# Kernel optimization log

Hardware: AMD Instinct MI355X
Metric: run time of the kernel (lower is better)

Reference implementation:

```python
import jax, jax.numpy as jnp
import numpy as np

N_EMBED = 384
HEAD_SIZE = 64
B, T = 128, 512


def rope(x):
    # Faithful to source: fres = 1/1000**(arange(0,dim,2)//dim) -> integer
    # floor-div makes the exponent all zeros, so fres == 1 everywhere.
    Bx, Tx, D = x.shape
    half = D // 2
    fres = jnp.ones((half,), dtype=jnp.float32)
    ang = jnp.arange(Tx, dtype=jnp.float32)[:, None] * fres[None, :]  # (T, half)
    cos, sin = jnp.cos(ang), jnp.sin(ang)
    xr = x.reshape(Bx, Tx, half, 2)
    xe, xo = xr[..., 0], xr[..., 1]
    oe = xe * cos - xo * sin
    oo = xe * sin + xo * cos
    return jnp.stack([oe, oo], axis=-1).reshape(Bx, Tx, D)


def setup_inputs() -> dict:
    key = jax.random.key(0)
    ks = jax.random.split(key, 7)
    s = 1.0 / np.sqrt(N_EMBED)
    return {
        "x": jax.random.normal(ks[0], (B, T, N_EMBED), dtype=jnp.float32),
        "wq": jax.random.uniform(ks[1], (N_EMBED, HEAD_SIZE), jnp.float32, -s, s),
        "bq": jax.random.uniform(ks[2], (HEAD_SIZE,), jnp.float32, -s, s),
        "wk": jax.random.uniform(ks[3], (N_EMBED, HEAD_SIZE), jnp.float32, -s, s),
        "bk": jax.random.uniform(ks[4], (HEAD_SIZE,), jnp.float32, -s, s),
        "wv": jax.random.uniform(ks[5], (N_EMBED, HEAD_SIZE), jnp.float32, -s, s),
        "bv": jax.random.uniform(ks[6], (HEAD_SIZE,), jnp.float32, -s, s),
    }


def reference(x, wq, bq, wk, bk, wv, bv):
    Bx, Tx, C = x.shape  # C = n_embed; scale uses C per the source (not head_size)
    q = rope(x @ wq + bq)
    k = rope(x @ wk + bk)
    wei = jnp.einsum("bqd,bkd->bqk", q, k) * (C ** -0.5)  # (B, T, T)
    causal = jnp.tril(jnp.ones((Tx, Tx), dtype=bool))
    wei = jnp.where(causal, wei, -jnp.inf)
    wei = jax.nn.softmax(wei, axis=-1)
    v = x @ wv + bv
    return jnp.einsum("bqk,bkd->bqd", wei, v)
```

## Files before the change

kernel.cpp:

```cpp
#include <hip/hip_runtime.h>

#define TSEQ 512
#define NB   128
#define CDIM 384
#define HD   64
#define QSCALE 0.051031036307982884f
#define MBIAS  8.0f

typedef _Float16 half8  __attribute__((ext_vector_type(8)));
typedef _Float16 half4  __attribute__((ext_vector_type(4)));
typedef float    floatx4 __attribute__((ext_vector_type(4)));

typedef __attribute__((address_space(3))) unsigned int lds_u32;
typedef const __attribute__((address_space(1))) unsigned int g_u32;

__device__ __forceinline__ void load_lds16(const void* g, void* l) {
    __builtin_amdgcn_global_load_lds((g_u32*)g, (lds_u32*)l, 16, 0, 0);
}

__global__ void prep_w(const float* __restrict__ wq, const float* __restrict__ wk,
                       const float* __restrict__ wv, _Float16* __restrict__ Wp)
{
    int i = blockIdx.x * 256 + threadIdx.x;
    if (i >= 3 * CDIM * HD) return;
    int c    = i / 6144;  int r  = i - c * 6144;
    int kblk = r / 1536;  int r2 = r - kblk * 1536;
    int n    = r2 >> 3;   int kin = r2 & 7;
    int k    = c * 32 + kblk * 8 + kin;
    int mat  = n / 64;    int col = n - mat * 64;
    const float* w = (mat == 0) ? wq : ((mat == 1) ? wk : wv);
    Wp[i] = (_Float16)w[k * HD + col];
}

__global__ __launch_bounds__(256) void qkv_gemm(
    const float* __restrict__ x, const _Float16* __restrict__ Wp,
    const float* __restrict__ bq, const float* __restrict__ bk,
    const float* __restrict__ bv,
    _Float16* __restrict__ Qw, _Float16* __restrict__ Kw,
    _Float16* __restrict__ Vtw, int b0)
{
    __shared__ __align__(16) float    xs[2][64 * 32];
    __shared__ __align__(16) _Float16 wsb[2][6144];

    const int tid  = threadIdx.x;
    const int wave = tid >> 6;
    const int lane = tid & 63;
    const int l16  = lane & 15;
    const int quad = lane >> 4;

    const int row0 = blockIdx.x * 64;
    const size_t rowg = (size_t)b0 * TSEQ + row0;

    const int xr = lane >> 3;
    const int xu = lane & 7;
    size_t xoff[2];
#pragma unroll
    for (int i = 0; i < 2; ++i) {
        const int m = (wave * 2 + i) * 8 + xr;
        xoff[i] = (rowg + m) * CDIM + (size_t)((xu ^ xr) << 2);
    }
    int woff[3];
#pragma unroll
    for (int i = 0; i < 3; ++i) woff[i] = (wave * 3 + i) * 512 + lane * 8;

    floatx4 acc[12];
#pragma unroll
    for (int i = 0; i < 12; ++i)
#pragma unroll
        for (int r = 0; r < 4; ++r) acc[i][r] = 0.f;

#define STAGE(cc, bi) do {                                                    \
    _Pragma("unroll")                                                         \
    for (int i_ = 0; i_ < 2; ++i_)                                            \
        load_lds16(x + xoff[i_] + (cc) * 32,                                  \
                   (char*)&xs[bi][0] + (wave * 2 + i_) * 1024);               \
    _Pragma("unroll")                                                         \
    for (int i_ = 0; i_ < 3; ++i_)                                            \
        load_lds16(Wp + (cc) * 6144 + woff[i_],                               \
                   (char*)&wsb[bi][0] + (wave * 3 + i_) * 1024);              \
} while (0)

    STAGE(0, 0);
    __syncthreads();

#pragma unroll
    for (int c = 0; c < 12; ++c) {
        if (c < 11) STAGE(c + 1, (c + 1) & 1);

        const float*    xb = xs[c & 1];
        const _Float16* wb = wsb[c & 1];
        const int m  = wave * 16 + l16;
        const int mh = l16 & 7;
        const int j0 = quad * 2;
        floatx4 a0 = *(const floatx4*)(xb + m * 32 + ((j0 ^ mh) << 2));
        floatx4 a1 = *(const floatx4*)(xb + m * 32 + (((j0 + 1) ^ mh) << 2));
        half8 a;
#pragma unroll
        for (int jj = 0; jj < 8; ++jj)
            a[jj] = (_Float16)(jj < 4 ? a0[jj] : a1[jj - 4]);
        const _Float16* bp = wb + ((size_t)quad * 192 + l16) * 8;
#pragma unroll
        for (int i = 0; i < 12; ++i) {
            half8 bb = *(const half8*)(bp + i * 128);
            acc[i] = __builtin_amdgcn_mfma_f32_16x16x32_f16(a, bb, acc[i], 0, 0, 0);
        }
        __syncthreads();
    }
#undef STAGE

    float bq4[4], bk4[4], bv4[4];
#pragma unroll
    for (int s4 = 0; s4 < 4; ++s4) {
        const int cc = s4 * 16 + l16;
        bq4[s4] = bq[cc]; bk4[s4] = bk[cc]; bv4[s4] = bv[cc];
    }
    const int t00  = (row0 & (TSEQ - 1)) + wave * 16 + quad * 4;
    const int bidx = row0 >> 9;
    const int rowb = row0 + wave * 16 + quad * 4;

#pragma unroll
    for (int r = 0; r < 4; ++r) {
        const int t = t00 + r;
        const float st = sinf((float)t);
        const float ct = cosf((float)t);
        const int row = rowb + r;
#pragma unroll
        for (int s4 = 0; s4 < 4; ++s4) {
            const int cc = s4 * 16 + l16;
            float vq = acc[s4][r] + bq4[s4];
            float pq = __shfl_xor(vq, 1);
            vq = (cc & 1) ? (pq * st + vq * ct) : (vq * ct - pq * st);
            Qw[(size_t)row * HD + cc] = (_Float16)(vq * QSCALE);
            float vk = acc[4 + s4][r] + bk4[s4];
            float pk = __shfl_xor(vk, 1);
            vk = (cc & 1) ? (pk * st + vk * ct) : (vk * ct - pk * st);
            Kw[(size_t)row * HD + cc] = (_Float16)vk;
        }
    }
#pragma unroll
    for (int s4 = 0; s4 < 4; ++s4) {
        const int cc = s4 * 16 + l16;
        half4 vpack;
#pragma unroll
        for (int r = 0; r < 4; ++r) vpack[r] = (_Float16)(acc[8 + s4][r] + bv4[s4]);
        *(half4*)(Vtw + ((size_t)bidx * HD + cc) * TSEQ + t00) = vpack;
    }
}

__global__ __launch_bounds__(256) void attn_kernel(
    const _Float16* __restrict__ Qw, const _Float16* __restrict__ Kw,
    const _Float16* __restrict__ Vtw, float* __restrict__ out, int b0)
{
    int bx, bl;
    {
        const int lin = blockIdx.y * 8 + blockIdx.x;
        if ((gridDim.y & 7) == 0) {
            const int per = gridDim.y >> 3;
            const int xcd = lin & 7;
            const int k2  = lin >> 3;
            bl = xcd * per + (k2 >> 3);
            bx = k2 & 7;
        } else { bx = blockIdx.x; bl = blockIdx.y; }
    }
    const int tid  = threadIdx.x;
    const int wave = tid >> 6;
    const int lane = tid & 63;
    const int l16  = lane & 15;
    const int quad = lane >> 4;

    const int pr  = bx * 2 + (wave & 1);
    const int h   = wave >> 1;
    const int qA  = pr * 16;
    const int qB  = (31 - pr) * 16;
    const int jdA = pr >> 2;
    const int jdB = (31 - pr) >> 2;

    __shared__ __align__(16) _Float16 pbuf[4][16][72];
    __shared__ __align__(16) floatx4  mbuf[2][10][64];

    const _Float16* Qb = Qw  + (size_t)bl * TSEQ * HD;
    const _Float16* Kb = Kw  + (size_t)bl * TSEQ * HD;
    const _Float16* Vb = Vtw + (size_t)bl * HD * TSEQ;

    half8 aQA0 = *(const half8*)(Qb + (size_t)(qA + l16) * HD + quad * 8);
    half8 aQA1 = *(const half8*)(Qb + (size_t)(qA + l16) * HD + 32 + quad * 8);
    half8 aQB0 = *(const half8*)(Qb + (size_t)(qB + l16) * HD + quad * 8);
    half8 aQB1 = *(const half8*)(Qb + (size_t)(qB + l16) * HD + 32 + quad * 8);

    half8 ones;
#pragma unroll
    for (int jj = 0; jj < 8; ++jj) ones[jj] = (_Float16)1.f;

    floatx4 accO[8], accL[2];
#pragma unroll
    for (int i = 0; i < 8; ++i)
#pragma unroll
        for (int r = 0; r < 4; ++r) accO[i][r] = 0.f;
#pragma unroll
    for (int s = 0; s < 2; ++s)
#pragma unroll
        for (int r = 0; r < 4; ++r) accL[s][r] = 0.f;

    for (int j = h; j <= jdB; j += 2) {
        const int kb = j * 64;

        half8 bK0[4], bK1[4], bV0[4], bV1[4];
#pragma unroll
        for (int s4 = 0; s4 < 4; ++s4) {
            const _Float16* kp = Kb + (size_t)(kb + s4 * 16 + l16) * HD + quad * 8;
            bK0[s4] = *(const half8*)(kp);
            bK1[s4] = *(const half8*)(kp + 32);
            const _Float16* vp = Vb + (size_t)(s4 * 16 + l16) * TSEQ + kb + quad * 8;
            bV0[s4] = *(const half8*)(vp);
            bV1[s4] = *(const half8*)(vp + 32);
        }

        if (j <= jdA) {
            floatx4 st4[4];
            __builtin_amdgcn_s_setprio(1);
#pragma unroll
            for (int s4 = 0; s4 < 4; ++s4) {
#pragma unroll
                for (int r = 0; r < 4; ++r) st4[s4][r] = 0.f;
                st4[s4] = __builtin_amdgcn_mfma_f32_16x16x32_f16(bK0[s4], aQA0, st4[s4], 0, 0, 0);
                st4[s4] = __builtin_amdgcn_mfma_f32_16x16x32_f16(bK1[s4], aQA1, st4[s4], 0, 0, 0);
            }
            __builtin_amdgcn_s_setprio(0);
            const int qrow = qA + l16;
#pragma unroll
            for (int s4 = 0; s4 < 4; ++s4) {
                half4 w;
#pragma unroll
                for (int r = 0; r < 4; ++r) {
                    float p = __expf(fminf(st4[s4][r], 18.f) - MBIAS);
                    if (j == jdA) {
                        const int kcol = kb + s4 * 16 + quad * 4 + r;
                        if (kcol > qrow) p = 0.f;
                    }
                    w[r] = (_Float16)p;
                }
                *(half4*)(&pbuf[wave][l16][s4 * 16 + quad * 4]) = w;
            }
            half8 aP0 = *(const half8*)(&pbuf[wave][l16][quad * 8]);
            half8 aP1 = *(const half8*)(&pbuf[wave][l16][32 + quad * 8]);
            __builtin_amdgcn_s_setprio(1);
#pragma unroll
            for (int s4 = 0; s4 < 4; ++s4) {
                accO[s4] = __builtin_amdgcn_mfma_f32_16x16x32_f16(aP0, bV0[s4], accO[s4], 0, 0, 0);
                accO[s4] = __builtin_amdgcn_mfma_f32_16x16x32_f16(aP1, bV1[s4], accO[s4], 0, 0, 0);
            }
            accL[0] = __builtin_amdgcn_mfma_f32_16x16x32_f16(aP0, ones, accL[0], 0, 0, 0);
            accL[0] = __builtin_amdgcn_mfma_f32_16x16x32_f16(aP1, ones, accL[0], 0, 0, 0);
            __builtin_amdgcn_s_setprio(0);
        }

        {
            floatx4 st4[4];
            __builtin_amdgcn_s_setprio(1);
#pragma unroll
            for (int s4 = 0; s4 < 4; ++s4) {
#pragma unroll
                for (int r = 0; r < 4; ++r) st4[s4][r] = 0.f;
                st4[s4] = __builtin_amdgcn_mfma_f32_16x16x32_f16(bK0[s4], aQB0, st4[s4], 0, 0, 0);
                st4[s4] = __builtin_amdgcn_mfma_f32_16x16x32_f16(bK1[s4], aQB1, st4[s4], 0, 0, 0);
            }
            __builtin_amdgcn_s_setprio(0);
            const int qrow = qB + l16;
#pragma unroll
            for (int s4 = 0; s4 < 4; ++s4) {
                half4 w;
#pragma unroll
                for (int r = 0; r < 4; ++r) {
                    float p = __expf(fminf(st4[s4][r], 18.f) - MBIAS);
                    if (j == jdB) {
                        const int kcol = kb + s4 * 16 + quad * 4 + r;
                        if (kcol > qrow) p = 0.f;
                    }
                    w[r] = (_Float16)p;
                }
                *(half4*)(&pbuf[wave][l16][s4 * 16 + quad * 4]) = w;
            }
            half8 aP0 = *(const half8*)(&pbuf[wave][l16][quad * 8]);
            half8 aP1 = *(const half8*)(&pbuf[wave][l16][32 + quad * 8]);
            __builtin_amdgcn_s_setprio(1);
#pragma unroll
            for (int s4 = 0; s4 < 4; ++s4) {
                accO[4 + s4] = __builtin_amdgcn_mfma_f32_16x16x32_f16(aP0, bV0[s4], accO[4 + s4], 0, 0, 0);
                accO[4 + s4] = __builtin_amdgcn_mfma_f32_16x16x32_f16(aP1, bV1[s4], accO[4 + s4], 0, 0, 0);
            }
            accL[1] = __builtin_amdgcn_mfma_f32_16x16x32_f16(aP0, ones, accL[1], 0, 0, 0);
            accL[1] = __builtin_amdgcn_mfma_f32_16x16x32_f16(aP1, ones, accL[1], 0, 0, 0);
            __builtin_amdgcn_s_setprio(0);
        }
    }

    const int slot = wave & 1;
    if (h == 1) {
#pragma unroll
        for (int i = 0; i < 8; ++i) mbuf[slot][i][lane] = accO[i];
        mbuf[slot][8][lane] = accL[0];
        mbuf[slot][9][lane] = accL[1];
    }
    __syncthreads();
    if (h == 1) return;

#pragma unroll
    for (int i = 0; i < 8; ++i) {
        floatx4 t = mbuf[slot][i][lane];
#pragma unroll
        for (int r = 0; r < 4; ++r) accO[i][r] += t[r];
    }
    {
        floatx4 t8 = mbuf[slot][8][lane];
        floatx4 t9 = mbuf[slot][9][lane];
#pragma unroll
        for (int r = 0; r < 4; ++r) { accL[0][r] += t8[r]; accL[1][r] += t9[r]; }
    }

#pragma unroll
    for (int s = 0; s < 2; ++s) {
        const int qbase = (s == 0) ? qA : qB;
        float inv[4];
#pragma unroll
        for (int r = 0; r < 4; ++r) inv[r] = 1.f / accL[s][r];
#pragma unroll
        for (int s4 = 0; s4 < 4; ++s4) {
            const int dcol = s4 * 16 + l16;
#pragma unroll
            for (int r = 0; r < 4; ++r) {
                const int qr = qbase + quad * 4 + r;
                out[((size_t)(b0 + bl) * TSEQ + qr) * HD + dcol] =
                    accO[s * 4 + s4][r] * inv[r];
            }
        }
    }
}

extern "C" void kernel_launch(void* const* d_in, const int* in_sizes, int n_in,
                              void* d_out, int out_size, void* d_ws, size_t ws_size,
                              hipStream_t stream)
{
    char* ws = (char*)d_ws;
    _Float16* Wp = (_Float16*)ws;
    char* qkv_base = ws + 147456;

    const size_t per_b = (size_t)3 * TSEQ * HD * sizeof(_Float16);
    size_t avail = (ws_size > (size_t)147456) ? ws_size - 147456 : per_b;
    int nbc = (int)(avail / per_b);
    if (nbc > NB) nbc = NB;
    if (nbc < 1)  nbc = 1;

    const size_t chunk_elems = (size_t)nbc * TSEQ * HD;
    _Float16* Qw  = (_Float16*)qkv_base;
    _Float16* Kw  = Qw + chunk_elems;
    _Float16* Vtw = Kw + chunk_elems;

    prep_w<<<dim3((3 * CDIM * HD + 255) / 256), dim3(256), 0, stream>>>(
        (const float*)d_in[1], (const float*)d_in[3], (const float*)d_in[5], Wp);

    for (int b0 = 0; b0 < NB; b0 += nbc) {
        const int nb = (NB - b0 < nbc) ? (NB - b0) : nbc;
        qkv_gemm<<<dim3(nb * 8), dim3(256), 0, stream>>>(
            (const float*)d_in[0], Wp, (const float*)d_in[2], (const float*)d_in[4],
            (const float*)d_in[6], Qw, Kw, Vtw, b0);
        attn_kernel<<<dim3(8, nb), dim3(256), 0, stream>>>(
            Qw, Kw, Vtw, (float*)d_out, b0);
    }
}
```

Before: 210.6 us.

## Double tile rows in QKV GEMM with register x loads; prefetch K/V in attention

The QKV GEMM now computes 128 rows per block, two 16-row groups per wave. x is loaded straight into registers with a register double buffer instead of staging through LDS, and W is staged through a triple-buffered LDS ring using explicit vmcnt waits and raw barriers. The attention loop is software-pipelined so the K/V fragments for the next tile are loaded while the current one is processed, and attn_kernel gets a launch bound asking for two blocks per CU. This is meant to hide global load latency and reuse W across more rows, at the cost of more registers and fewer GEMM blocks.

Result: slower. 220.5 us (+4.7%).

```diff
diff --git a/kernel.cpp b/kernel.cpp
--- a/kernel.cpp
+++ b/kernel.cpp
@@ -39,8 +39,7 @@
     _Float16* __restrict__ Qw, _Float16* __restrict__ Kw,
     _Float16* __restrict__ Vtw, int b0)
 {
-    __shared__ __align__(16) float    xs[2][64 * 32];
-    __shared__ __align__(16) _Float16 wsb[2][6144];
+    __shared__ __align__(16) _Float16 wsb[3][6144];
 
     const int tid  = threadIdx.x;
     const int wave = tid >> 6;
@@ -48,65 +47,77 @@
     const int l16  = lane & 15;
     const int quad = lane >> 4;
 
-    const int row0 = blockIdx.x * 64;
+    const int row0 = blockIdx.x * 128;
     const size_t rowg = (size_t)b0 * TSEQ + row0;
 
-    const int xr = lane >> 3;
-    const int xu = lane & 7;
-    size_t xoff[2];
-#pragma unroll
-    for (int i = 0; i < 2; ++i) {
-        const int m = (wave * 2 + i) * 8 + xr;
-        xoff[i] = (rowg + m) * CDIM + (size_t)((xu ^ xr) << 2);
-    }
     int woff[3];
 #pragma unroll
     for (int i = 0; i < 3; ++i) woff[i] = (wave * 3 + i) * 512 + lane * 8;
 
-    floatx4 acc[12];
-#pragma unroll
-    for (int i = 0; i < 12; ++i)
-#pragma unroll
-        for (int r = 0; r < 4; ++r) acc[i][r] = 0.f;
-
-#define STAGE(cc, bi) do {                                                    \
+    const float* xp[2];
+#pragma unroll
+    for (int g = 0; g < 2; ++g)
+        xp[g] = x + (rowg + wave * 32 + g * 16 + l16) * CDIM + quad * 8;
+
+    floatx4 acc[2][12];
+#pragma unroll
+    for (int g = 0; g < 2; ++g)
+#pragma unroll
+        for (int i = 0; i < 12; ++i)
+#pragma unroll
+            for (int r = 0; r < 4; ++r) acc[g][i][r] = 0.f;
+
+    floatx4 xA[2][2], xB[2][2];
+
+#define WSTAGE(cc) do { _Pragma("unroll")                                     \
+    for (int i_ = 0; i_ < 3; ++i_)                                            \
+        load_lds16(Wp + (size_t)(cc) * 6144 + woff[i_],                       \
+                   (char*)&wsb[(cc) % 3][0] + (wave * 3 + i_) * 1024);        \
+} while (0)
+
+#define XLOAD(cc, S) do { _Pragma("unroll")                                   \
+    for (int g_ = 0; g_ < 2; ++g_) {                                          \
+        S[g_][0] = *(const floatx4*)(xp[g_] + (cc) * 32);                     \
+        S[g_][1] = *(const floatx4*)(xp[g_] + (cc) * 32 + 4);                 \
+    }                                                                         \
+} while (0)
+
+#define CHUNK(cc, CUR, NXT, VM) do {                                          \
+    if ((cc) + 2 < 12) WSTAGE((cc) + 2);                                      \
+    if ((cc) + 1 < 12) XLOAD((cc) + 1, NXT);                                  \
+    asm volatile("s_waitcnt vmcnt(" VM ")" ::: "memory");                     \
+    half8 aF[2];                                                              \
     _Pragma("unroll")                                                         \
-    for (int i_ = 0; i_ < 2; ++i_)                                            \
-        load_lds16(x + xoff[i_] + (cc) * 32,                                  \
-                   (char*)&xs[bi][0] + (wave * 2 + i_) * 1024);               \
+    for (int g_ = 0; g_ < 2; ++g_) {                                          \
+        _Pragma("unroll")                                                     \
+        for (int jj = 0; jj < 8; ++jj)                                        \
+            aF[g_][jj] = (_Float16)(jj < 4 ? CUR[g_][0][jj]                   \
+                                           : CUR[g_][1][jj - 4]);             \
+    }                                                                         \
+    const _Float16* bp = &wsb[(cc) % 3][0] + ((size_t)quad * 192 + l16) * 8;  \
     _Pragma("unroll")                                                         \
-    for (int i_ = 0; i_ < 3; ++i_)                                            \
-        load_lds16(Wp + (cc) * 6144 + woff[i_],                               \
-                   (char*)&wsb[bi][0] + (wave * 3 + i_) * 1024);              \
-} while (0)
-
-    STAGE(0, 0);
-    __syncthreads();
-
-#pragma unroll
-    for (int c = 0; c < 12; ++c) {
-        if (c < 11) STAGE(c + 1, (c + 1) & 1);
-
-        const float*    xb = xs[c & 1];
-        const _Float16* wb = wsb[c & 1];
-        const int m  = wave * 16 + l16;
-        const int mh = l16 & 7;
-        const int j0 = quad * 2;
-        floatx4 a0 = *(const floatx4*)(xb + m * 32 + ((j0 ^ mh) << 2));
-        floatx4 a1 = *(const floatx4*)(xb + m * 32 + (((j0 + 1) ^ mh) << 2));
-        half8 a;
-#pragma unroll
-        for (int jj = 0; jj < 8; ++jj)
-            a[jj] = (_Float16)(jj < 4 ? a0[jj] : a1[jj - 4]);
-        const _Float16* bp = wb + ((size_t)quad * 192 + l16) * 8;
-#pragma unroll
-        for (int i = 0; i < 12; ++i) {
-            half8 bb = *(const half8*)(bp + i * 128);
-            acc[i] = __builtin_amdgcn_mfma_f32_16x16x32_f16(a, bb, acc[i], 0, 0, 0);
-        }
-        __syncthreads();
-    }
-#undef STAGE
+    for (int i_ = 0; i_ < 12; ++i_) {                                         \
+        half8 bb = *(const half8*)(bp + i_ * 128);                            \
+        acc[0][i_] = __builtin_amdgcn_mfma_f32_16x16x32_f16(aF[0], bb, acc[0][i_], 0, 0, 0); \
+        acc[1][i_] = __builtin_amdgcn_mfma_f32_16x16x32_f16(aF[1], bb, acc[1][i_], 0, 0, 0); \
+    }                                                                         \
+    __builtin_amdgcn_s_barrier();                                             \
+} while (0)
+
+    WSTAGE(0); WSTAGE(1); XLOAD(0, xA);
+    asm volatile("s_waitcnt vmcnt(7)" ::: "memory");
+    __builtin_amdgcn_s_barrier();
+
+    CHUNK(0,  xA, xB, "7");  CHUNK(1,  xB, xA, "7");
+    CHUNK(2,  xA, xB, "7");  CHUNK(3,  xB, xA, "7");
+    CHUNK(4,  xA, xB, "7");  CHUNK(5,  xB, xA, "7");
+    CHUNK(6,  xA, xB, "7");  CHUNK(7,  xB, xA, "7");
+    CHUNK(8,  xA, xB, "7");  CHUNK(9,  xB, xA, "7");
+    CHUNK(10, xA, xB, "4");  CHUNK(11, xB, xA, "0");
+
+#undef CHUNK
+#undef XLOAD
+#undef WSTAGE
 
     float bq4[4], bk4[4], bv4[4];
 #pragma unroll
@@ -114,40 +125,45 @@
         const int cc = s4 * 16 + l16;
         bq4[s4] = bq[cc]; bk4[s4] = bk[cc]; bv4[s4] = bv[cc];
     }
-    const int t00  = (row0 & (TSEQ - 1)) + wave * 16 + quad * 4;
     const int bidx = row0 >> 9;
-    const int rowb = row0 + wave * 16 + quad * 4;
-
-#pragma unroll
-    for (int r = 0; r < 4; ++r) {
-        const int t = t00 + r;
-        const float st = sinf((float)t);
-        const float ct = cosf((float)t);
-        const int row = rowb + r;
+    const int rb   = wave * 32 + quad * 4;
+
+#pragma unroll
+    for (int g = 0; g < 2; ++g) {
+        const int t00 = (row0 & (TSEQ - 1)) + rb + g * 16;
+        const int r00 = row0 + rb + g * 16;
+#pragma unroll
+        for (int r = 0; r < 4; ++r) {
+            const int t = t00 + r;
+            const float st = sinf((float)t);
+            const float ct = cosf((float)t);
+            const int row = r00 + r;
+#pragma unroll
+            for (int s4 = 0; s4 < 4; ++s4) {
+                const int cc = s4 * 16 + l16;
+                float vq = acc[g][s4][r] + bq4[s4];
+                float pq = __shfl_xor(vq, 1);
+                vq = (cc & 1) ? (pq * st + vq * ct) : (vq * ct - pq * st);
+                Qw[(size_t)row * HD + cc] = (_Float16)(vq * QSCALE);
+                float vk = acc[g][4 + s4][r] + bk4[s4];
+                float pk = __shfl_xor(vk, 1);
+                vk = (cc & 1) ? (pk * st + vk * ct) : (vk * ct - pk * st);
+                Kw[(size_t)row * HD + cc] = (_Float16)vk;
+            }
+        }
 #pragma unroll
         for (int s4 = 0; s4 < 4; ++s4) {
             const int cc = s4 * 16 + l16;
-            float vq = acc[s4][r] + bq4[s4];
-            float pq = __shfl_xor(vq, 1);
-            vq = (cc & 1) ? (pq * st + vq * ct) : (vq * ct - pq * st);
-            Qw[(size_t)row * HD + cc] = (_Float16)(vq * QSCALE);
-            float vk = acc[4 + s4][r] + bk4[s4];
-            float pk = __shfl_xor(vk, 1);
-            vk = (cc & 1) ? (pk * st + vk * ct) : (vk * ct - pk * st);
-            Kw[(size_t)row * HD + cc] = (_Float16)vk;
+            half4 vpack;
+#pragma unroll
+            for (int r = 0; r < 4; ++r)
+                vpack[r] = (_Float16)(acc[g][8 + s4][r] + bv4[s4]);
+            *(half4*)(Vtw + ((size_t)bidx * HD + cc) * TSEQ + t00) = vpack;
         }
     }
-#pragma unroll
-    for (int s4 = 0; s4 < 4; ++s4) {
-        const int cc = s4 * 16 + l16;
-        half4 vpack;
-#pragma unroll
-        for (int r = 0; r < 4; ++r) vpack[r] = (_Float16)(acc[8 + s4][r] + bv4[s4]);
-        *(half4*)(Vtw + ((size_t)bidx * HD + cc) * TSEQ + t00) = vpack;
-    }
-}
-
-__global__ __launch_bounds__(256) void attn_kernel(
+}
+
+__global__ __launch_bounds__(256, 2) void attn_kernel(
     const _Float16* __restrict__ Qw, const _Float16* __restrict__ Kw,
     const _Float16* __restrict__ Vtw, float* __restrict__ out, int b0)
 {
@@ -201,98 +217,111 @@
 #pragma unroll
         for (int r = 0; r < 4; ++r) accL[s][r] = 0.f;
 
-    for (int j = h; j <= jdB; j += 2) {
-        const int kb = j * 64;
-
-        half8 bK0[4], bK1[4], bV0[4], bV1[4];
-#pragma unroll
-        for (int s4 = 0; s4 < 4; ++s4) {
-            const _Float16* kp = Kb + (size_t)(kb + s4 * 16 + l16) * HD + quad * 8;
-            bK0[s4] = *(const half8*)(kp);
-            bK1[s4] = *(const half8*)(kp + 32);
-            const _Float16* vp = Vb + (size_t)(s4 * 16 + l16) * TSEQ + kb + quad * 8;
-            bV0[s4] = *(const half8*)(vp);
-            bV1[s4] = *(const half8*)(vp + 32);
-        }
-
-        if (j <= jdA) {
-            floatx4 st4[4];
-            __builtin_amdgcn_s_setprio(1);
-#pragma unroll
-            for (int s4 = 0; s4 < 4; ++s4) {
-#pragma unroll
-                for (int r = 0; r < 4; ++r) st4[s4][r] = 0.f;
-                st4[s4] = __builtin_amdgcn_mfma_f32_16x16x32_f16(bK0[s4], aQA0, st4[s4], 0, 0, 0);
-                st4[s4] = __builtin_amdgcn_mfma_f32_16x16x32_f16(bK1[s4], aQA1, st4[s4], 0, 0, 0);
-            }
-            __builtin_amdgcn_s_setprio(0);
-            const int qrow = qA + l16;
-#pragma unroll
-            for (int s4 = 0; s4 < 4; ++s4) {
-                half4 w;
-#pragma unroll
-                for (int r = 0; r < 4; ++r) {
-                    float p = __expf(fminf(st4[s4][r], 18.f) - MBIAS);
-                    if (j == jdA) {
-                        const int kcol = kb + s4 * 16 + quad * 4 + r;
-                        if (kcol > qrow) p = 0.f;
-                    }
-                    w[r] = (_Float16)p;
-                }
-                *(half4*)(&pbuf[wave][l16][s4 * 16 + quad * 4]) = w;
-            }
-            half8 aP0 = *(const half8*)(&pbuf[wave][l16][quad * 8]);
-            half8 aP1 = *(const half8*)(&pbuf[wave][l16][32 + quad * 8]);
-            __builtin_amdgcn_s_setprio(1);
-#pragma unroll
-            for (int s4 = 0; s4 < 4; ++s4) {
-                accO[s4] = __builtin_amdgcn_mfma_f32_16x16x32_f16(aP0, bV0[s4], accO[s4], 0, 0, 0);
-                accO[s4] = __builtin_amdgcn_mfma_f32_16x16x32_f16(aP1, bV1[s4], accO[s4], 0, 0, 0);
-            }
-            accL[0] = __builtin_amdgcn_mfma_f32_16x16x32_f16(aP0, ones, accL[0], 0, 0, 0);
-            accL[0] = __builtin_amdgcn_mfma_f32_16x16x32_f16(aP1, ones, accL[0], 0, 0, 0);
-            __builtin_amdgcn_s_setprio(0);
-        }
-
-        {
-            floatx4 st4[4];
-            __builtin_amdgcn_s_setprio(1);
-#pragma unroll
-            for (int s4 = 0; s4 < 4; ++s4) {
-#pragma unroll
-                for (int r = 0; r < 4; ++r) st4[s4][r] = 0.f;
-                st4[s4] = __builtin_amdgcn_mfma_f32_16x16x32_f16(bK0[s4], aQB0, st4[s4], 0, 0, 0);
-                st4[s4] = __builtin_amdgcn_mfma_f32_16x16x32_f16(bK1[s4], aQB1, st4[s4], 0, 0, 0);
-            }
-            __builtin_amdgcn_s_setprio(0);
-            const int qrow = qB + l16;
-#pragma unroll
-            for (int s4 = 0; s4 < 4; ++s4) {
-                half4 w;
-#pragma unroll
-                for (int r = 0; r < 4; ++r) {
-                    float p = __expf(fminf(st4[s4][r], 18.f) - MBIAS);
-                    if (j == jdB) {
-                        const int kcol = kb + s4 * 16 + quad * 4 + r;
-                        if (kcol > qrow) p = 0.f;
-                    }
-                    w[r] = (_Float16)p;
-                }
-                *(half4*)(&pbuf[wave][l16][s4 * 16 + quad * 4]) = w;
-            }
-            half8 aP0 = *(const half8*)(&pbuf[wave][l16][quad * 8]);
-            half8 aP1 = *(const half8*)(&pbuf[wave][l16][32 + quad * 8]);
-            __builtin_amdgcn_s_setprio(1);
-#pragma unroll
-            for (int s4 = 0; s4 < 4; ++s4) {
-                accO[4 + s4] = __builtin_amdgcn_mfma_f32_16x16x32_f16(aP0, bV0[s4], accO[4 + s4], 0, 0, 0);
-                accO[4 + s4] = __builtin_amdgcn_mfma_f32_16x16x32_f16(aP1, bV1[s4], accO[4 + s4], 0, 0, 0);
-            }
-            accL[1] = __builtin_amdgcn_mfma_f32_16x16x32_f16(aP0, ones, accL[1], 0, 0, 0);
-            accL[1] = __builtin_amdgcn_mfma_f32_16x16x32_f16(aP1, ones, accL[1], 0, 0, 0);
-            __builtin_amdgcn_s_setprio(0);
-        }
-    }
+    half8 cK0[4], cK1[4], cV0[4], cV1[4];
+    half8 nK0[4], nK1[4], nV0[4], nV1[4];
+
+#define KVLOAD(jv, K0, K1, V0, V1) do {                                       \
+    const int kb_ = ((jv) * 64 > TSEQ - 64) ? (TSEQ - 64) : (jv) * 64;        \
+    _Pragma("unroll")                                                         \
+    for (int s4 = 0; s4 < 4; ++s4) {                                          \
+        const _Float16* kp = Kb + (size_t)(kb_ + s4 * 16 + l16) * HD + quad * 8; \
+        K0[s4] = *(const half8*)(kp);                                         \
+        K1[s4] = *(const half8*)(kp + 32);                                    \
+        const _Float16* vp = Vb + (size_t)(s4 * 16 + l16) * TSEQ + kb_ + quad * 8; \
+        V0[s4] = *(const half8*)(vp);                                         \
+        V1[s4] = *(const half8*)(vp + 32);                                    \
+    }                                                                         \
+} while (0)
+
+#define BODY(jv, K0, K1, V0, V1) do {                                         \
+    const int kb = (jv) * 64;                                                 \
+    if ((jv) <= jdA) {                                                        \
+        floatx4 st4[4];                                                       \
+        __builtin_amdgcn_s_setprio(1);                                        \
+        _Pragma("unroll")                                                     \
+        for (int s4 = 0; s4 < 4; ++s4) {                                      \
+            _Pragma("unroll")                                                 \
+            for (int r = 0; r < 4; ++r) st4[s4][r] = 0.f;                     \
+            st4[s4] = __builtin_amdgcn_mfma_f32_16x16x32_f16(K0[s4], aQA0, st4[s4], 0, 0, 0); \
+            st4[s4] = __builtin_amdgcn_mfma_f32_16x16x32_f16(K1[s4], aQA1, st4[s4], 0, 0, 0); \
+        }                                                                     \
+        __builtin_amdgcn_s_setprio(0);                                        \
+        const int qrow = qA + l16;                                            \
+        _Pragma("unroll")                                                     \
+        for (int s4 = 0; s4 < 4; ++s4) {                                      \
+            half4 w;                                                          \
+            _Pragma("unroll")                                                 \
+            for (int r = 0; r < 4; ++r) {                                     \
+                float p = __expf(fminf(st4[s4][r], 18.f) - MBIAS);            \
+                if ((jv) == jdA) {                                            \
+                    const int kcol = kb + s4 * 16 + quad * 4 + r;             \
+                    if (kcol > qrow) p = 0.f;                                 \
+                }                                                             \
+                w[r] = (_Float16)p;                                           \
+            }                                                                 \
+            *(half4*)(&pbuf[wave][l16][s4 * 16 + quad * 4]) = w;              \
+        }                                                                     \
+        half8 aP0 = *(const half8*)(&pbuf[wave][l16][quad * 8]);              \
+        half8 aP1 = *(const half8*)(&pbuf[wave][l16][32 + quad * 8]);         \
+        __builtin_amdgcn_s_setprio(1);                                        \
+        _Pragma("unroll")                                                     \
+        for (int s4 = 0; s4 < 4; ++s4) {                                      \
+            accO[s4] = __builtin_amdgcn_mfma_f32_16x16x32_f16(aP0, V0[s4], accO[s4], 0, 0, 0); \
+            accO[s4] = __builtin_amdgcn_mfma_f32_16x16x32_f16(aP1, V1[s4], accO[s4], 0, 0, 0); \
+        }                                                                     \
+        accL[0] = __builtin_amdgcn_mfma_f32_16x16x32_f16(aP0, ones, accL[0], 0, 0, 0); \
+        accL[0] = __builtin_amdgcn_mfma_f32_16x16x32_f16(aP1, ones, accL[0], 0, 0, 0); \
+        __builtin_amdgcn_s_setprio(0);                                        \
+    }                                                                         \
+    {                                                                         \
+        floatx4 st4[4];                                                       \
+        __builtin_amdgcn_s_setprio(1);                                        \
+        _Pragma("unroll")                                                     \
+        for (int s4 = 0; s4 < 4; ++s4) {                                      \
+            _Pragma("unroll")                                                 \
+            for (int r = 0; r < 4; ++r) st4[s4][r] = 0.f;                     \
+            st4[s4] = __builtin_amdgcn_mfma_f32_16x16x32_f16(K0[s4], aQB0, st4[s4], 0, 0, 0); \
+            st4[s4] = __builtin_amdgcn_mfma_f32_16x16x32_f16(K1[s4], aQB1, st4[s4], 0, 0, 0); \
+        }                                                                     \
+        __builtin_amdgcn_s_setprio(0);                                        \
+        const int qrow = qB + l16;                                            \
+        _Pragma("unroll")                                                     \
+        for (int s4 = 0; s4 < 4; ++s4) {                                      \
+            half4 w;                                                          \
+            _Pragma("unroll")                                                 \
+            for (int r = 0; r < 4; ++r) {                                     \
+                float p = __expf(fminf(st4[s4][r], 18.f) - MBIAS);            \
+                if ((jv) == jdB) {                                            \
+                    const int kcol = kb + s4 * 16 + quad * 4 + r;             \
+                    if (kcol > qrow) p = 0.f;                                 \
+                }                                                             \
+                w[r] = (_Float16)p;                                           \
+            }                                                                 \
+            *(half4*)(&pbuf[wave][l16][s4 * 16 + quad * 4]) = w;              \
+        }                                                                     \
+        half8 aP0 = *(const half8*)(&pbuf[wave][l16][quad * 8]);              \
+        half8 aP1 = *(const half8*)(&pbuf[wave][l16][32 + quad * 8]);         \
+        __builtin_amdgcn_s_setprio(1);                                        \
+        _Pragma("unroll")                                                     \
+        for (int s4 = 0; s4 < 4; ++s4) {                                      \
+            accO[4 + s4] = __builtin_amdgcn_mfma_f32_16x16x32_f16(aP0, V0[s4], accO[4 + s4], 0, 0, 0); \
+            accO[4 + s4] = __builtin_amdgcn_mfma_f32_16x16x32_f16(aP1, V1[s4], accO[4 + s4], 0, 0, 0); \
+        }                                                                     \
+        accL[1] = __builtin_amdgcn_mfma_f32_16x16x32_f16(aP0, ones, accL[1], 0, 0, 0); \
+        accL[1] = __builtin_amdgcn_mfma_f32_16x16x32_f16(aP1, ones, accL[1], 0, 0, 0); \
+        __builtin_amdgcn_s_setprio(0);                                        \
+    }                                                                         \
+} while (0)
+
+    KVLOAD(h, cK0, cK1, cV0, cV1);
+    for (int j = h; j <= jdB; j += 4) {
+        KVLOAD(j + 2, nK0, nK1, nV0, nV1);
+        BODY(j, cK0, cK1, cV0, cV1);
+        KVLOAD(j + 4, cK0, cK1, cV0, cV1);
+        if (j + 2 <= jdB) BODY(j + 2, nK0, nK1, nV0, nV1);
+    }
+#undef BODY
+#undef KVLOAD
 
     const int slot = wave & 1;
     if (h == 1) {
@@ -360,7 +389,7 @@
 
     for (int b0 = 0; b0 < NB; b0 += nbc) {
         const int nb = (NB - b0 < nbc) ? (NB - b0) : nbc;
-        qkv_gemm<<<dim3(nb * 8), dim3(256), 0, stream>>>(
+        qkv_gemm<<<dim3(nb * 4), dim3(256), 0, stream>>>(
             (const float*)d_in[0], Wp, (const float*)d_in[2], (const float*)d_in[4],
             (const float*)d_in[6], Qw, Kw, Vtw, b0);
         attn_kernel<<<dim3(8, nb), dim3(256), 0, stream>>>(
```

## Load x directly to registers, double M tile, triple-buffer weights in qkv_gemm

Applied to the files above, without the earlier changes.

The QKV projection kernel now gives each block 128 rows instead of 64. Each wave reads its x fragments straight from global memory into registers, prefetched one chunk ahead, rather than staging them through LDS. Weight tiles go through a three-deep LDS ring, with explicit vmcnt waits and raw barriers in place of __syncthreads. Each weight fragment read from LDS now feeds two MFMAs, which cuts LDS traffic and sync overhead. The cost is more accumulator registers, half as many blocks, and hand-tuned wait counts that must match the load order exactly.

After: 211.2 us. No clear change (+0.3%).

```diff
diff --git a/kernel.cpp b/kernel.cpp
--- a/kernel.cpp
+++ b/kernel.cpp
@@ -39,8 +39,7 @@
     _Float16* __restrict__ Qw, _Float16* __restrict__ Kw,
     _Float16* __restrict__ Vtw, int b0)
 {
-    __shared__ __align__(16) float    xs[2][64 * 32];
-    __shared__ __align__(16) _Float16 wsb[2][6144];
+    __shared__ __align__(16) _Float16 wsb[3][6144];
 
     const int tid  = threadIdx.x;
     const int wave = tid >> 6;
@@ -48,65 +47,77 @@
     const int l16  = lane & 15;
     const int quad = lane >> 4;
 
-    const int row0 = blockIdx.x * 64;
+    const int row0 = blockIdx.x * 128;
     const size_t rowg = (size_t)b0 * TSEQ + row0;
 
-    const int xr = lane >> 3;
-    const int xu = lane & 7;
-    size_t xoff[2];
-#pragma unroll
-    for (int i = 0; i < 2; ++i) {
-        const int m = (wave * 2 + i) * 8 + xr;
-        xoff[i] = (rowg + m) * CDIM + (size_t)((xu ^ xr) << 2);
-    }
     int woff[3];
 #pragma unroll
     for (int i = 0; i < 3; ++i) woff[i] = (wave * 3 + i) * 512 + lane * 8;
 
-    floatx4 acc[12];
-#pragma unroll
-    for (int i = 0; i < 12; ++i)
-#pragma unroll
-        for (int r = 0; r < 4; ++r) acc[i][r] = 0.f;
-
-#define STAGE(cc, bi) do {                                                    \
+    const float* xp[2];
+#pragma unroll
+    for (int g = 0; g < 2; ++g)
+        xp[g] = x + (rowg + wave * 32 + g * 16 + l16) * CDIM + quad * 8;
+
+    floatx4 acc[2][12];
+#pragma unroll
+    for (int g = 0; g < 2; ++g)
+#pragma unroll
+        for (int i = 0; i < 12; ++i)
+#pragma unroll
+            for (int r = 0; r < 4; ++r) acc[g][i][r] = 0.f;
+
+    floatx4 xA[2][2], xB[2][2];
+
+#define WSTAGE(cc) do { _Pragma("unroll")                                     \
+    for (int i_ = 0; i_ < 3; ++i_)                                            \
+        load_lds16(Wp + (size_t)(cc) * 6144 + woff[i_],                       \
+                   (char*)&wsb[(cc) % 3][0] + (wave * 3 + i_) * 1024);        \
+} while (0)
+
+#define XLOAD(cc, S) do { _Pragma("unroll")                                   \
+    for (int g_ = 0; g_ < 2; ++g_) {                                          \
+        S[g_][0] = *(const floatx4*)(xp[g_] + (cc) * 32);                     \
+        S[g_][1] = *(const floatx4*)(xp[g_] + (cc) * 32 + 4);                 \
+    }                                                                         \
+} while (0)
+
+#define CHUNK(cc, CUR, NXT, VM) do {                                          \
+    if ((cc) + 2 < 12) WSTAGE((cc) + 2);                                      \
+    if ((cc) + 1 < 12) XLOAD((cc) + 1, NXT);                                  \
+    asm volatile("s_waitcnt vmcnt(" VM ")" ::: "memory");                     \
+    half8 aF[2];                                                              \
     _Pragma("unroll")                                                         \
-    for (int i_ = 0; i_ < 2; ++i_)                                            \
-        load_lds16(x + xoff[i_] + (cc) * 32,                                  \
-                   (char*)&xs[bi][0] + (wave * 2 + i_) * 1024);               \
+    for (int g_ = 0; g_ < 2; ++g_) {                                          \
+        _Pragma("unroll")                                                     \
+        for (int jj = 0; jj < 8; ++jj)                                        \
+            aF[g_][jj] = (_Float16)(jj < 4 ? CUR[g_][0][jj]                   \
+                                           : CUR[g_][1][jj - 4]);             \
+    }                                                                         \
+    const _Float16* bp = &wsb[(cc) % 3][0] + ((size_t)quad * 192 + l16) * 8;  \
     _Pragma("unroll")                                                         \
-    for (int i_ = 0; i_ < 3; ++i_)                                            \
-        load_lds16(Wp + (cc) * 6144 + woff[i_],                               \
-                   (char*)&wsb[bi][0] + (wave * 3 + i_) * 1024);              \
+    for (int i_ = 0; i_ < 12; ++i_) {                                         \
+        half8 bb = *(const half8*)(bp + i_ * 128);                            \
+        acc[0][i_] = __builtin_amdgcn_mfma_f32_16x16x32_f16(aF[0], bb, acc[0][i_], 0, 0, 0); \
+        acc[1][i_] = __builtin_amdgcn_mfma_f32_16x16x32_f16(aF[1], bb, acc[1][i_], 0, 0, 0); \
+    }                                                                         \
+    __builtin_amdgcn_s_barrier();                                             \
 } while (0)
 
-    STAGE(0, 0);
-    __syncthreads();
-
-#pragma unroll
-    for (int c = 0; c < 12; ++c) {
-        if (c < 11) STAGE(c + 1, (c + 1) & 1);
-
-        const float*    xb = xs[c & 1];
-        const _Float16* wb = wsb[c & 1];
-        const int m  = wave * 16 + l16;
-        const int mh = l16 & 7;
-        const int j0 = quad * 2;
-        floatx4 a0 = *(const floatx4*)(xb + m * 32 + ((j0 ^ mh) << 2));
-        floatx4 a1 = *(const floatx4*)(xb + m * 32 + (((j0 + 1) ^ mh) << 2));
-        half8 a;
-#pragma unroll
-        for (int jj = 0; jj < 8; ++jj)
-            a[jj] = (_Float16)(jj < 4 ? a0[jj] : a1[jj - 4]);
-        const _Float16* bp = wb + ((size_t)quad * 192 + l16) * 8;
-#pragma unroll
-        for (int i = 0; i < 12; ++i) {
-            half8 bb = *(const half8*)(bp + i * 128);
-            acc[i] = __builtin_amdgcn_mfma_f32_16x16x32_f16(a, bb, acc[i], 0, 0, 0);
-        }
-        __syncthreads();
-    }
-#undef STAGE
+    WSTAGE(0); WSTAGE(1); XLOAD(0, xA);
+    asm volatile("s_waitcnt vmcnt(7)" ::: "memory");
+    __builtin_amdgcn_s_barrier();
+
+    CHUNK(0,  xA, xB, "7");  CHUNK(1,  xB, xA, "7");
+    CHUNK(2,  xA, xB, "7");  CHUNK(3,  xB, xA, "7");
+    CHUNK(4,  xA, xB, "7");  CHUNK(5,  xB, xA, "7");
+    CHUNK(6,  xA, xB, "7");  CHUNK(7,  xB, xA, "7");
+    CHUNK(8,  xA, xB, "7");  CHUNK(9,  xB, xA, "7");
+    CHUNK(10, xA, xB, "4");  CHUNK(11, xB, xA, "0");
+
+#undef CHUNK
+#undef XLOAD
+#undef WSTAGE
 
     float bq4[4], bk4[4], bv4[4];
 #pragma unroll
@@ -114,36 +125,41 @@
         const int cc = s4 * 16 + l16;
         bq4[s4] = bq[cc]; bk4[s4] = bk[cc]; bv4[s4] = bv[cc];
     }
-    const int t00  = (row0 & (TSEQ - 1)) + wave * 16 + quad * 4;
     const int bidx = row0 >> 9;
-    const int rowb = row0 + wave * 16 + quad * 4;
-
-#pragma unroll
-    for (int r = 0; r < 4; ++r) {
-        const int t = t00 + r;
-        const float st = sinf((float)t);
-        const float ct = cosf((float)t);
-        const int row = rowb + r;
+    const int rb   = wave * 32 + quad * 4;
+
+#pragma unroll
+    for (int g = 0; g < 2; ++g) {
+        const int t00 = (row0 & (TSEQ - 1)) + rb + g * 16;
+        const int r00 = row0 + rb + g * 16;
+#pragma unroll
+        for (int r = 0; r < 4; ++r) {
+            const int t = t00 + r;
+            const float st = sinf((float)t);
+            const float ct = cosf((float)t);
+            const int row = r00 + r;
+#pragma unroll
+            for (int s4 = 0; s4 < 4; ++s4) {
+                const int cc = s4 * 16 + l16;
+                float vq = acc[g][s4][r] + bq4[s4];
+                float pq = __shfl_xor(vq, 1);
+                vq = (cc & 1) ? (pq * st + vq * ct) : (vq * ct - pq * st);
+                Qw[(size_t)row * HD + cc] = (_Float16)(vq * QSCALE);
+                float vk = acc[g][4 + s4][r] + bk4[s4];
+                float pk = __shfl_xor(vk, 1);
+                vk = (cc & 1) ? (pk * st + vk * ct) : (vk * ct - pk * st);
+                Kw[(size_t)row * HD + cc] = (_Float16)vk;
+            }
+        }
 #pragma unroll
         for (int s4 = 0; s4 < 4; ++s4) {
             const int cc = s4 * 16 + l16;
-            float vq = acc[s4][r] + bq4[s4];
-            float pq = __shfl_xor(vq, 1);
-            vq = (cc & 1) ? (pq * st + vq * ct) : (vq * ct - pq * st);
-            Qw[(size_t)row * HD + cc] = (_Float16)(vq * QSCALE);
-            float vk = acc[4 + s4][r] + bk4[s4];
-            float pk = __shfl_xor(vk, 1);
-            vk = (cc & 1) ? (pk * st + vk * ct) : (vk * ct - pk * st);
-            Kw[(size_t)row * HD + cc] = (_Float16)vk;
-        }
-    }
-#pragma unroll
-    for (int s4 = 0; s4 < 4; ++s4) {
-        const int cc = s4 * 16 + l16;
-        half4 vpack;
-#pragma unroll
-        for (int r = 0; r < 4; ++r) vpack[r] = (_Float16)(acc[8 + s4][r] + bv4[s4]);
-        *(half4*)(Vtw + ((size_t)bidx * HD + cc) * TSEQ + t00) = vpack;
+            half4 vpack;
+#pragma unroll
+            for (int r = 0; r < 4; ++r)
+                vpack[r] = (_Float16)(acc[g][8 + s4][r] + bv4[s4]);
+            *(half4*)(Vtw + ((size_t)bidx * HD + cc) * TSEQ + t00) = vpack;
+        }
     }
 }
 
@@ -360,7 +376,7 @@
 
     for (int b0 = 0; b0 < NB; b0 += nbc) {
         const int nb = (NB - b0 < nbc) ? (NB - b0) : nbc;
-        qkv_gemm<<<dim3(nb * 8), dim3(256), 0, stream>>>(
+        qkv_gemm<<<dim3(nb * 4), dim3(256), 0, stream>>>(
             (const float*)d_in[0], Wp, (const float*)d_in[2], (const float*)d_in[4],
             (const float*)d_in[6], Qw, Kw, Vtw, b0);
         attn_kernel<<<dim3(8, nb), dim3(256), 0, stream>>>(
```
